# Optimization experiments

Hardware: AMD Instinct MI355X
Metric: run time of the kernel (lower is better)

The kernel has to match this reference:

```python
import jax, jax.numpy as jnp
import numpy as np

B, L, H, E = 32, 128, 768, 64


def setup_inputs() -> dict:
    key = jax.random.key(0)
    ks = jax.random.split(key, 9)
    bert = jax.random.normal(ks[0], (B, L, H), jnp.float32)
    dep = jax.random.normal(ks[1], (B, L, L, E), jnp.float32)
    adj = jax.random.bernoulli(ks[2], 0.06, (B, L, L)).astype(jnp.int32)
    adj = adj.at[:, :, L - 1].set(0)  # avoid torch.roll wrap pairing edge case
    asp_start = jax.random.randint(ks[3], (B,), 1, L // 2)
    span = jax.random.randint(ks[4], (B,), 0, 4)
    asp_end = jnp.minimum(asp_start + span, L - 2)
    sc = 1.0 / np.sqrt(H).astype(np.float32)
    Wz = jax.random.normal(ks[5], (H, H), jnp.float32) * sc
    bz = jnp.zeros((H,), jnp.float32)
    wa = jax.random.normal(ks[6], (2 * H + E,), jnp.float32) * sc
    ba = jnp.zeros((), jnp.float32)
    Wf = jax.random.normal(ks[7], (H, H + E), jnp.float32) * sc
    Wh = jax.random.normal(ks[8], (H, 2 * H), jnp.float32) * sc
    return dict(bert_hidden_states=bert, dep_type_adj=dep, deprel_adj=adj,
                asp_start=asp_start, asp_end=asp_end,
                Wz=Wz, bz=bz, wa=wa, ba=ba, Wf=Wf, Wh=Wh)


def _forward(bert, dep, adj, asp_start, asp_end, Wz, bz, wa, ba, Wf, Wh):
    # z = z_linear(bert); zs[b, j] = z[b, j+1] (rolled-mask offset: adjacency idx j -> token j+1)
    z = bert @ Wz.T + bz
    zs = jnp.roll(z, -1, axis=1)                      # [B,L,H]
    wa_i, wa_j, wa_e = wa[:H], wa[H:2 * H], wa[2 * H:]
    s_i = zs @ wa_i                                    # [B,L] current-aspect term
    s_j = zs @ wa_j                                    # [B,L] neighbor term
    s_e = jnp.einsum('bije,e->bij', dep, wa_e)         # [B,L,L] dep-embed term
    score = jax.nn.leaky_relu(s_i[:, :, None] + s_j[:, None, :] + s_e + ba, 0.01)
    nb_mask = adj > 0                                  # [B,L,L]
    attn = jax.nn.softmax(jnp.where(nb_mask, score, -1e9), axis=-1)
    attn = jnp.where(nb_mask, attn, 0.0)
    # dep_type_fusion([neighbor, dep]) = zs @ Wf_z^T + dep @ Wf_e^T; weighted sum over j
    A = zs @ Wf[:, :H].T                               # [B,L,H]
    D = jnp.einsum('bij,bije->bie', attn, dep)         # [B,L,E]
    neighbor_repr = jnp.einsum('bij,bjh->bih', attn, A) + D @ Wf[:, H:].T  # [B,L,H]
    # w_h([neighbor_repr, current_asp_repr])
    temp = neighbor_repr @ Wh[:, :H].T + zs @ Wh[:, H:].T                   # [B,L,H]
    pos = jnp.arange(L)
    asp_valid = (pos[None, :] >= asp_start[:, None]) & (pos[None, :] <= asp_end[:, None])
    upd = asp_valid & nb_mask.any(-1)                  # update only aspects with >=1 neighbor
    # result for adjacency index i is written to token position i+1
    out = jnp.where(jnp.roll(upd, 1, axis=1)[:, :, None], jnp.roll(temp, 1, axis=1), bert)
    return out


def reference(bert_hidden_states, dep_type_adj, deprel_adj, asp_start, asp_end, Wz, bz, wa, ba, Wf, Wh):
    return _forward(bert_hidden_states, dep_type_adj, deprel_adj, asp_start, asp_end,
                    Wz, bz, wa, ba, Wf, Wh)
```

## Files before the change

kernel.cpp:

```cpp
#include <hip/hip_runtime.h>
#include <math.h>

#define NB 32
#define NL 128
#define NH 768
#define NE 64

#define OFF_ASLOT   32784
#define OFF_AIDX    49168
#define OFF_NASP    49680
#define OFF_AJCNT   49808
#define OFF_AJIDX   50320
#define OFF_RMAP    148624
#define OFF_BZD     155280
#define OFF_YB      155296
#define OFF_DG      548512
#define OFF_YP      581280
#define OFF_ZSAP    2154144
#define OFF_NBR     3727008
#define OFF_VIP     6872736
#define OFF_VJP     6897312

__global__ __launch_bounds__(256) void kA(
    const int* __restrict__ adj, const int* __restrict__ asp_s, const int* __restrict__ asp_e,
    const float* __restrict__ Wz, const float* __restrict__ wa, const float* __restrict__ bz,
    const float* __restrict__ bert,
    int* __restrict__ aspect_slot, int* __restrict__ aspect_idx, int* __restrict__ nasp,
    int* __restrict__ aj_cnt, int* __restrict__ aj_idx, int* __restrict__ row_map,
    float* __restrict__ viP, float* __restrict__ vjP, float* __restrict__ bzd,
    float* __restrict__ out) {
  int blk = blockIdx.x, tid = threadIdx.x;
  if (blk < 32) {
    int b = blk;
    __shared__ int asp_flag[128];
    __shared__ int s_aidx[4];
    __shared__ int s_nasp;
    if (tid < 128) {
      const int* arow = adj + ((size_t)(b * 128 + tid)) * 128;
      int any = 0;
      for (int j = 0; j < 128; j += 4) {
        int4 v = *(const int4*)(arow + j);
        any |= v.x | v.y | v.z | v.w;
      }
      int s0 = asp_s[b], e0 = asp_e[b];
      asp_flag[tid] = (tid >= s0 && tid <= e0 && any > 0) ? 1 : 0;
      aspect_slot[b * 128 + tid] = -1;
    }
    if (tid >= 128 && tid < 132) row_map[b * 4 + (tid - 128)] = b * 128;
    __syncthreads();
    if (tid == 0) {
      int n = 0;
      for (int i = 0; i < 128; ++i)
        if (asp_flag[i] && n < 4) s_aidx[n++] = i;
      s_nasp = n;
      nasp[b] = n;
    }
    __syncthreads();
    int w = tid >> 6, l = tid & 63;
    if (w < s_nasp) {
      int a = s_aidx[w];
      if (l == 0) {
        aspect_idx[b * 4 + w] = a;
        aspect_slot[b * 128 + a] = w;
        row_map[b * 4 + w] = b * 128 + a;
      }
      const int* ar = adj + ((size_t)(b * 128 + a)) * 128;
      int v0 = (ar[l] > 0) ? 1 : 0;
      int v1 = (ar[l + 64] > 0) ? 1 : 0;
      unsigned long long m0 = __ballot(v0);
      unsigned long long m1 = __ballot(v1);
      unsigned long long below = (1ull << l) - 1ull;
      int c0 = __popcll(m0 & below);
      int c1 = __popcll(m0) + __popcll(m1 & below);
      int* dst = aj_idx + (size_t)(b * 4 + w) * 128;
      if (v0) dst[c0] = l;
      if (v1) dst[c1] = l + 64;
      if (l == 0) aj_cnt[b * 4 + w] = __popcll(m0) + __popcll(m1);
    }
  } else if (blk < 56) {
    int idx = blk - 32;
    int kb = idx % 3, hb = idx / 3;
    int k = kb * 256 + tid;
    int h0 = hb * 96;
    float ai = 0.f, aj = 0.f;
#pragma unroll 8
    for (int h = h0; h < h0 + 96; ++h) {
      float w = Wz[(size_t)h * 768 + k];
      ai += w * wa[h];
      aj += w * wa[768 + h];
    }
    viP[hb * 768 + k] = ai;
    vjP[hb * 768 + k] = aj;
  } else if (blk == 56) {
    if (tid < 64) {
      float bi = 0.f, bj = 0.f;
#pragma unroll
      for (int q = 0; q < 12; ++q) {
        float bv = bz[q * 64 + tid];
        bi += bv * wa[q * 64 + tid];
        bj += bv * wa[768 + q * 64 + tid];
      }
#pragma unroll
      for (int d = 32; d; d >>= 1) { bi += __shfl_xor(bi, d, 64); bj += __shfl_xor(bj, d, 64); }
      if (tid == 0) { bzd[0] = bi; bzd[1] = bj; }
    }
  } else {
    int row = blk - 57;
    int b = row >> 7, i = row & 127;
    __shared__ int s_upd;
    if (tid == 0) s_upd = 0;
    __syncthreads();
    if (i > 0) {
      int ip = i - 1;
      int s0 = asp_s[b], e0 = asp_e[b];
      if (ip >= s0 && ip <= e0 && tid < 64) {
        const int2* ar = (const int2*)(adj + ((size_t)(b * 128 + ip)) * 128);
        int2 v = ar[tid];
        unsigned long long m = __ballot((v.x | v.y) != 0);
        if (tid == 0 && m != 0ull) s_upd = 1;
      }
    }
    __syncthreads();
    if (tid < 192) {
      float4 v = make_float4(0.f, 0.f, 0.f, 0.f);
      if (!s_upd) v = ((const float4*)bert)[(size_t)row * 192 + tid];
      ((float4*)out)[(size_t)row * 192 + tid] = v;
    }
  }
}

__global__ __launch_bounds__(256) void kB(
    const float* __restrict__ dep, const float* __restrict__ bert,
    const float* __restrict__ wa, const float* __restrict__ ba,
    const float* __restrict__ viP, const float* __restrict__ vjP, const float* __restrict__ bzd,
    const float* __restrict__ Wz, const float* __restrict__ bz,
    const int* __restrict__ nasp, const int* __restrict__ aspect_idx,
    const int* __restrict__ aj_cnt, const int* __restrict__ aj_idx,
    const int* __restrict__ row_map,
    float* __restrict__ YB, float* __restrict__ DG, float* __restrict__ zsap) {
  int blk = blockIdx.x, tid = threadIdx.x;
  if (blk < 32) {
    int b = blk;
    int na = nasp[b];
    if (na == 0) return;
    __shared__ float vis[768];
    __shared__ float vjs[768];
    __shared__ float att[4][128];
    __shared__ float sjs[4][128];
    __shared__ float sis[4];
    __shared__ int jl[4][128];
    __shared__ int aidx[4];
    __shared__ int ajc[4];
    __shared__ float wae[64];
    if (tid < 4) { aidx[tid] = aspect_idx[b * 4 + tid]; ajc[tid] = aj_cnt[b * 4 + tid]; }
    if (tid < 64) wae[tid] = wa[1536 + tid];
    for (int q = tid; q < 512; q += 256) jl[q >> 7][q & 127] = aj_idx[b * 512 + q];
    for (int q = tid; q < 768; q += 256) {
      float a = 0.f, c = 0.f;
#pragma unroll
      for (int hb = 0; hb < 8; ++hb) { a += viP[hb * 768 + q]; c += vjP[hb * 768 + q]; }
      vis[q] = a;
      vjs[q] = c;
    }
    __syncthreads();
    int w = tid >> 6, l = tid & 63;
    float bzd0 = bzd[0], bzd1 = bzd[1];
    int offs[5];
    {
      int o = 0;
      for (int w2 = 0; w2 < 4; ++w2) { offs[w2] = o; if (w2 < na) o += 1 + ajc[w2]; }
      offs[4] = o;
    }
    for (int p = w; p < offs[4]; p += 4) {
      int w2 = 0;
      if (p >= offs[1]) w2 = 1;
      if (p >= offs[2]) w2 = 2;
      if (p >= offs[3]) w2 = 3;
      int idx = p - offs[w2];
      int row = (idx == 0) ? aidx[w2] : jl[w2][idx - 1];
      const float* br = bert + (size_t)(b * 128 + ((row + 1) & 127)) * 768;
      float acc = 0.f;
      if (idx == 0) {
#pragma unroll
        for (int q = 0; q < 12; ++q) acc += br[q * 64 + l] * vis[q * 64 + l];
      } else {
#pragma unroll
        for (int q = 0; q < 12; ++q) acc += br[q * 64 + l] * vjs[q * 64 + l];
      }
#pragma unroll
      for (int d = 32; d; d >>= 1) acc += __shfl_xor(acc, d, 64);
      if (l == 0) {
        if (idx == 0) sis[w2] = acc + bzd0;
        else sjs[w2][idx - 1] = acc + bzd1;
      }
    }
    __syncthreads();
    if (w >= na) return;
    int a = aidx[w], cj = ajc[w];
    float sib = sis[w] + ba[0];
    const float* depa = dep + ((size_t)(b * 128 + a)) * 128 * 64;
    float sc0 = -INFINITY, sc1 = -INFINITY;
    for (int t = l; t < cj; t += 64) {
      int j = jl[w][t];
      const float4* dp = (const float4*)(depa + (size_t)j * 64);
      float se = 0.f;
#pragma unroll
      for (int q = 0; q < 16; ++q) {
        float4 v = dp[q];
        se += v.x * wae[4 * q] + v.y * wae[4 * q + 1] + v.z * wae[4 * q + 2] + v.w * wae[4 * q + 3];
      }
      float sc = sib + sjs[w][t] + se;
      sc = (sc >= 0.f) ? sc : 0.01f * sc;
      if (t < 64) sc0 = sc; else sc1 = sc;
    }
    float mx = fmaxf(sc0, sc1);
#pragma unroll
    for (int d = 32; d; d >>= 1) mx = fmaxf(mx, __shfl_xor(mx, d, 64));
    float p0 = expf(sc0 - mx), p1 = expf(sc1 - mx);
    float sm = p0 + p1;
#pragma unroll
    for (int d = 32; d; d >>= 1) sm += __shfl_xor(sm, d, 64);
    float inv = 1.f / sm;
    if (l < cj) att[w][l] = p0 * inv;
    if (l + 64 < cj) att[w][l + 64] = p1 * inv;
    float y[12];
#pragma unroll
    for (int q = 0; q < 12; ++q) y[q] = 0.f;
    float dacc = 0.f;
    for (int t = 0; t < cj; ++t) {
      float at = att[w][t];
      int j = jl[w][t];
      const float* br = bert + (size_t)(b * 128 + ((j + 1) & 127)) * 768;
#pragma unroll
      for (int q = 0; q < 12; ++q) y[q] += at * br[q * 64 + l];
      dacc += at * depa[(size_t)j * 64 + l];
    }
    float* yr = YB + (size_t)(b * 4 + w) * 768;
#pragma unroll
    for (int q = 0; q < 12; ++q) yr[q * 64 + l] = y[q];
    DG[(b * 4 + w) * 64 + l] = dacc;
  } else {
    int idx = blk - 32;
    int kc = idx & 3, hc = (idx >> 2) % 3, bx = idx / 12;
    int s0 = bx * 4;
    __shared__ float Xs[4][192];
    if (tid < 192) {
      int r = tid / 48, c = tid - r * 48;
      int zrow = row_map[s0 + r];
      int bb = zrow >> 7, ii = zrow & 127;
      const float4* src = (const float4*)(bert + ((size_t)(bb * 128) + ((ii + 1) & 127)) * 768) + kc * 48;
      ((float4*)Xs[r])[c] = src[c];
    }
    __syncthreads();
    int h = hc * 256 + tid;
    const float4* wp = (const float4*)(Wz + (size_t)h * 768) + kc * 48;
    float accA[4] = {};
    float accB[4] = {};
#pragma unroll 6
    for (int k4 = 0; k4 < 24; ++k4) {
      float4 w0 = wp[k4];
      float4 w1 = wp[k4 + 24];
#pragma unroll
      for (int r = 0; r < 4; ++r) {
        float4 x0 = ((const float4*)Xs[r])[k4];
        float4 x1 = ((const float4*)Xs[r])[k4 + 24];
        accA[r] += x0.x * w0.x + x0.y * w0.y + x0.z * w0.z + x0.w * w0.w;
        accB[r] += x1.x * w1.x + x1.y * w1.y + x1.z * w1.z + x1.w * w1.w;
      }
    }
    float bzv = (kc == 0) ? bz[h] : 0.f;
#pragma unroll
    for (int r = 0; r < 4; ++r)
      zsap[((size_t)kc * 128 + s0 + r) * 768 + h] = accA[r] + accB[r] + bzv;
  }
}

__global__ __launch_bounds__(256) void kC(
    const float* __restrict__ YB, const float* __restrict__ DG, const float* __restrict__ zsap,
    const float* __restrict__ Wz, const float* __restrict__ bz,
    const float* __restrict__ Wf, const float* __restrict__ Wh,
    const int* __restrict__ row_map, const int* __restrict__ nasp,
    float* __restrict__ yp, float* __restrict__ NBR, float* __restrict__ out) {
  int blk = blockIdx.x, tid = threadIdx.x;
  __shared__ float Xs[4][192];
  if (blk < 384) {
    int kc = blk & 3, hc = (blk >> 2) % 3, bx = blk / 12;
    int s0 = bx * 4;
    if (tid < 192) {
      int r = tid / 48, c = tid - r * 48;
      const float4* src = (const float4*)(YB + (size_t)(s0 + r) * 768) + kc * 48;
      ((float4*)Xs[r])[c] = src[c];
    }
    __syncthreads();
    int h = hc * 256 + tid;
    const float4* wp = (const float4*)(Wz + (size_t)h * 768) + kc * 48;
    float accA[4] = {};
    float accB[4] = {};
#pragma unroll 6
    for (int k4 = 0; k4 < 24; ++k4) {
      float4 w0 = wp[k4];
      float4 w1 = wp[k4 + 24];
#pragma unroll
      for (int r = 0; r < 4; ++r) {
        float4 x0 = ((const float4*)Xs[r])[k4];
        float4 x1 = ((const float4*)Xs[r])[k4 + 24];
        accA[r] += x0.x * w0.x + x0.y * w0.y + x0.z * w0.z + x0.w * w0.w;
        accB[r] += x1.x * w1.x + x1.y * w1.y + x1.z * w1.z + x1.w * w1.w;
      }
    }
    float bzv = (kc == 0) ? bz[h] : 0.f;
#pragma unroll
    for (int r = 0; r < 4; ++r)
      yp[((size_t)kc * 128 + s0 + r) * 768 + h] = accA[r] + accB[r] + bzv;
  } else if (blk < 768) {
    int idx = blk - 384;
    int kc2 = idx & 3, nc = (idx >> 2) % 3, g = idx / 12;
    if (tid < 192) {
      int r = tid / 48, c = tid - r * 48;
      int row = g * 4 + r;
      int Q = kc2 * 48 + c;
      float4 p0 = *((const float4*)(zsap + (size_t)row * 768) + Q);
      float4 p1 = *((const float4*)(zsap + ((size_t)128 + row) * 768) + Q);
      float4 p2 = *((const float4*)(zsap + ((size_t)256 + row) * 768) + Q);
      float4 p3 = *((const float4*)(zsap + ((size_t)384 + row) * 768) + Q);
      ((float4*)Xs[r])[c] = make_float4(p0.x + p1.x + p2.x + p3.x, p0.y + p1.y + p2.y + p3.y,
                                        p0.z + p1.z + p2.z + p3.z, p0.w + p1.w + p2.w + p3.w);
    }
    __syncthreads();
    int h = nc * 256 + tid;
    float acc[4] = {};
    const float4* wp = (const float4*)(Wh + (size_t)h * 1536 + 768 + kc2 * 192);
#pragma unroll 4
    for (int k4 = 0; k4 < 48; ++k4) {
      float4 wv = wp[k4];
#pragma unroll
      for (int r = 0; r < 4; ++r) {
        float4 xv = ((const float4*)Xs[r])[k4];
        acc[r] += xv.x * wv.x + xv.y * wv.y + xv.z * wv.z + xv.w * wv.w;
      }
    }
#pragma unroll
    for (int r = 0; r < 4; ++r) {
      int row = g * 4 + r;
      int b = row >> 2, s = row & 3;
      if (s < nasp[b]) {
        int orow = row_map[row] + 1;
        atomicAdd(&out[(size_t)orow * 768 + h], acc[r]);
      }
    }
  } else {
    int idx = blk - 768;
    int nc = idx % 3, g = idx / 3;
    if (tid < 64) {
      int r = tid / 16, c = tid - r * 16;
      ((float4*)Xs[r])[c] = *((const float4*)(DG + (size_t)(g * 4 + r) * 64) + c);
    }
    __syncthreads();
    int h = nc * 256 + tid;
    float acc[4] = {};
    const float4* wp = (const float4*)(Wf + (size_t)h * 832 + 768);
#pragma unroll
    for (int k4 = 0; k4 < 16; ++k4) {
      float4 wv = wp[k4];
#pragma unroll
      for (int r = 0; r < 4; ++r) {
        float4 xv = ((const float4*)Xs[r])[k4];
        acc[r] += xv.x * wv.x + xv.y * wv.y + xv.z * wv.z + xv.w * wv.w;
      }
    }
#pragma unroll
    for (int r = 0; r < 4; ++r)
      NBR[(size_t)(g * 4 + r) * 768 + h] = acc[r];
  }
}

__global__ __launch_bounds__(256) void kD(
    const float* __restrict__ yp, const float* __restrict__ Wf,
    float* __restrict__ NBR) {
  int blk = blockIdx.x, tid = threadIdx.x;
  int kc = blk & 3, nc = (blk >> 2) % 3, g = blk / 12;
  __shared__ float Xs[4][192];
  if (tid < 192) {
    int r = tid / 48, c = tid - r * 48;
    int row = g * 4 + r;
    int Q = kc * 48 + c;
    float4 p0 = *((const float4*)(yp + (size_t)row * 768) + Q);
    float4 p1 = *((const float4*)(yp + ((size_t)128 + row) * 768) + Q);
    float4 p2 = *((const float4*)(yp + ((size_t)256 + row) * 768) + Q);
    float4 p3 = *((const float4*)(yp + ((size_t)384 + row) * 768) + Q);
    ((float4*)Xs[r])[c] = make_float4(p0.x + p1.x + p2.x + p3.x, p0.y + p1.y + p2.y + p3.y,
                                      p0.z + p1.z + p2.z + p3.z, p0.w + p1.w + p2.w + p3.w);
  }
  __syncthreads();
  int h = nc * 256 + tid;
  float acc[4] = {};
  const float4* wp = (const float4*)(Wf + (size_t)h * 832 + kc * 192);
#pragma unroll 4
  for (int k4 = 0; k4 < 48; ++k4) {
    float4 wv = wp[k4];
#pragma unroll
    for (int r = 0; r < 4; ++r) {
      float4 xv = ((const float4*)Xs[r])[k4];
      acc[r] += xv.x * wv.x + xv.y * wv.y + xv.z * wv.z + xv.w * wv.w;
    }
  }
#pragma unroll
  for (int r = 0; r < 4; ++r)
    atomicAdd(&NBR[(size_t)(g * 4 + r) * 768 + h], acc[r]);
}

__global__ __launch_bounds__(256) void kE(
    const float* __restrict__ NBR, const float* __restrict__ Wh,
    const int* __restrict__ row_map, const int* __restrict__ nasp,
    float* __restrict__ out) {
  int blk = blockIdx.x, tid = threadIdx.x;
  int kc = blk & 3, nc = (blk >> 2) % 3, g = blk / 12;
  __shared__ float Xs[4][192];
  if (tid < 192) {
    int r = tid / 48, c = tid - r * 48;
    ((float4*)Xs[r])[c] = *((const float4*)(NBR + (size_t)(g * 4 + r) * 768 + kc * 192) + c);
  }
  __syncthreads();
  int h = nc * 256 + tid;
  float acc[4] = {};
  const float4* wp = (const float4*)(Wh + (size_t)h * 1536 + kc * 192);
#pragma unroll 4
  for (int k4 = 0; k4 < 48; ++k4) {
    float4 wv = wp[k4];
#pragma unroll
    for (int r = 0; r < 4; ++r) {
      float4 xv = ((const float4*)Xs[r])[k4];
      acc[r] += xv.x * wv.x + xv.y * wv.y + xv.z * wv.z + xv.w * wv.w;
    }
  }
#pragma unroll
  for (int r = 0; r < 4; ++r) {
    int row = g * 4 + r;
    int b = row >> 2, s = row & 3;
    if (s < nasp[b]) {
      int orow = row_map[row] + 1;
      atomicAdd(&out[(size_t)orow * 768 + h], acc[r]);
    }
  }
}

extern "C" void kernel_launch(void* const* d_in, const int* in_sizes, int n_in,
                              void* d_out, int out_size, void* d_ws, size_t ws_size,
                              hipStream_t stream) {
  const float* bert = (const float*)d_in[0];
  const float* dep  = (const float*)d_in[1];
  const int*   adj  = (const int*)d_in[2];
  const int*   asps = (const int*)d_in[3];
  const int*   aspe = (const int*)d_in[4];
  const float* Wz   = (const float*)d_in[5];
  const float* bz   = (const float*)d_in[6];
  const float* wa   = (const float*)d_in[7];
  const float* ba   = (const float*)d_in[8];
  const float* Wf   = (const float*)d_in[9];
  const float* Wh   = (const float*)d_in[10];
  float* out = (float*)d_out;
  char* ws = (char*)d_ws;

  int*   aspect_slot = (int*)(ws + OFF_ASLOT);
  int*   aspect_idx  = (int*)(ws + OFF_AIDX);
  int*   nasp        = (int*)(ws + OFF_NASP);
  int*   aj_cnt      = (int*)(ws + OFF_AJCNT);
  int*   aj_idx      = (int*)(ws + OFF_AJIDX);
  int*   row_map     = (int*)(ws + OFF_RMAP);
  float* bzd         = (float*)(ws + OFF_BZD);
  float* YB          = (float*)(ws + OFF_YB);
  float* DG          = (float*)(ws + OFF_DG);
  float* yp          = (float*)(ws + OFF_YP);
  float* zsap        = (float*)(ws + OFF_ZSAP);
  float* NBR         = (float*)(ws + OFF_NBR);
  float* viP         = (float*)(ws + OFF_VIP);
  float* vjP         = (float*)(ws + OFF_VJP);

  kA<<<4153, 256, 0, stream>>>(adj, asps, aspe, Wz, wa, bz, bert,
                               aspect_slot, aspect_idx, nasp, aj_cnt, aj_idx, row_map,
                               viP, vjP, bzd, out);
  kB<<<416, 256, 0, stream>>>(dep, bert, wa, ba, viP, vjP, bzd, Wz, bz,
                              nasp, aspect_idx, aj_cnt, aj_idx, row_map,
                              YB, DG, zsap);
  kC<<<864, 256, 0, stream>>>(YB, DG, zsap, Wz, bz, Wf, Wh, row_map, nasp, yp, NBR, out);
  kD<<<384, 256, 0, stream>>>(yp, Wf, NBR);
  kE<<<384, 256, 0, stream>>>(NBR, Wh, row_map, nasp, out);
}
```

Baseline: 86.80 us.

## Precompose weight matrices to collapse the Wz-Wf-Wh GEMM chain into one

Multiplies the linear weights together inside the kernels: Wt = Wf_z·Wz, We = Wh_n·Wt, plus a composed dep-embedding matrix and bias vectors. Each aspect row now needs one GEMM against We instead of the YB→Wz→Wf→Wh chain. This removes two kernel launches and the intermediate yp/NBR buffers. The cost is two dense 768×768×768 weight-weight GEMMs recomputed on every call, which is far more arithmetic than the original work on about 128 rows, and the changed summation order alters rounding.

```diff
diff --git a/kernel.cpp b/kernel.cpp
--- a/kernel.cpp
+++ b/kernel.cpp
@@ -15,19 +15,23 @@
 #define OFF_BZD     155280
 #define OFF_YB      155296
 #define OFF_DG      548512
-#define OFF_YP      581280
 #define OFF_ZSAP    2154144
-#define OFF_NBR     3727008
 #define OFF_VIP     6872736
 #define OFF_VJP     6897312
+#define OFF_WT      6921888
+#define OFF_WE      9281184
+#define OFF_WDT     11640480
+#define OFF_UP      12427296
+#define OFF_C1      12439584
 
 __global__ __launch_bounds__(256) void kA(
     const int* __restrict__ adj, const int* __restrict__ asp_s, const int* __restrict__ asp_e,
     const float* __restrict__ Wz, const float* __restrict__ wa, const float* __restrict__ bz,
-    const float* __restrict__ bert,
+    const float* __restrict__ bert, const float* __restrict__ Wf, const float* __restrict__ Wh,
     int* __restrict__ aspect_slot, int* __restrict__ aspect_idx, int* __restrict__ nasp,
     int* __restrict__ aj_cnt, int* __restrict__ aj_idx, int* __restrict__ row_map,
     float* __restrict__ viP, float* __restrict__ vjP, float* __restrict__ bzd,
+    float* __restrict__ uP, float* __restrict__ Wt, float* __restrict__ Wdtp,
     float* __restrict__ out) {
   int blk = blockIdx.x, tid = threadIdx.x;
   if (blk < 32) {
@@ -71,10 +75,10 @@
       unsigned long long m1 = __ballot(v1);
       unsigned long long below = (1ull << l) - 1ull;
       int c0 = __popcll(m0 & below);
-      int c1 = __popcll(m0) + __popcll(m1 & below);
+      int c1x = __popcll(m0) + __popcll(m1 & below);
       int* dst = aj_idx + (size_t)(b * 4 + w) * 128;
       if (v0) dst[c0] = l;
-      if (v1) dst[c1] = l + 64;
+      if (v1) dst[c1x] = l + 64;
       if (l == 0) aj_cnt[b * 4 + w] = __popcll(m0) + __popcll(m1);
     }
   } else if (blk < 56) {
@@ -104,8 +108,66 @@
       for (int d = 32; d; d >>= 1) { bi += __shfl_xor(bi, d, 64); bj += __shfl_xor(bj, d, 64); }
       if (tid == 0) { bzd[0] = bi; bzd[1] = bj; }
     }
+  } else if (blk < 69) {
+    int idx = blk - 57;
+    int hc = idx >> 2, kc = idx & 3;
+    int hh = hc * 256 + tid;
+    const float4* wp = (const float4*)(Wf + (size_t)hh * 832 + kc * 192);
+    const float4* bp = (const float4*)(bz + kc * 192);
+    float acc = 0.f;
+#pragma unroll 4
+    for (int k4 = 0; k4 < 48; ++k4) {
+      float4 w = wp[k4];
+      float4 b4 = bp[k4];
+      acc += w.x * b4.x + w.y * b4.y + w.z * b4.z + w.w * b4.w;
+    }
+    uP[kc * 768 + hh] = acc;
+  } else if (blk < 357) {
+    __shared__ float Xs8[8][768];
+    int idx = blk - 69;
+    int mg = idx / 3, nc = idx % 3;
+    int m0 = mg * 8;
+    for (int q = tid; q < 8 * 768; q += 256) {
+      int r = q / 768, c = q - r * 768;
+      Xs8[r][c] = Wf[(size_t)(m0 + r) * 832 + c];
+    }
+    __syncthreads();
+    int kg = tid & 63, wv = tid >> 6;
+    int mA = wv * 2, mB = wv * 2 + 1;
+    int n4 = nc * 256 + kg * 4;
+    float4 a0 = make_float4(0.f, 0.f, 0.f, 0.f);
+    float4 a1 = make_float4(0.f, 0.f, 0.f, 0.f);
+#pragma unroll 4
+    for (int h = 0; h < 768; ++h) {
+      float4 wz = *(const float4*)(Wz + (size_t)h * 768 + n4);
+      float x0 = Xs8[mA][h], x1 = Xs8[mB][h];
+      a0.x += x0 * wz.x; a0.y += x0 * wz.y; a0.z += x0 * wz.z; a0.w += x0 * wz.w;
+      a1.x += x1 * wz.x; a1.y += x1 * wz.y; a1.z += x1 * wz.z; a1.w += x1 * wz.w;
+    }
+    *(float4*)(Wt + (size_t)(m0 + mA) * 768 + n4) = a0;
+    *(float4*)(Wt + (size_t)(m0 + mB) * 768 + n4) = a1;
+  } else if (blk < 549) {
+    __shared__ float XsW[16][192];
+    int idx = blk - 357;
+    int mgd = idx >> 2, kc = idx & 3;
+    int m0 = mgd * 16;
+    for (int q = tid; q < 16 * 192; q += 256) {
+      int r = q / 192, c = q - r * 192;
+      XsW[r][c] = Wh[(size_t)(m0 + r) * 1536 + kc * 192 + c];
+    }
+    __syncthreads();
+    int e = tid & 63, mq = tid >> 6;
+    float acc[4] = {};
+    for (int h = 0; h < 192; ++h) {
+      float wf = Wf[(size_t)(kc * 192 + h) * 832 + 768 + e];
+#pragma unroll
+      for (int j = 0; j < 4; ++j) acc[j] += XsW[mq * 4 + j][h] * wf;
+    }
+#pragma unroll
+    for (int j = 0; j < 4; ++j)
+      Wdtp[((size_t)kc * 64 + e) * 768 + m0 + mq * 4 + j] = acc[j];
   } else {
-    int row = blk - 57;
+    int row = blk - 549;
     int b = row >> 7, i = row & 127;
     __shared__ int s_upd;
     if (tid == 0) s_upd = 0;
@@ -133,11 +195,13 @@
     const float* __restrict__ dep, const float* __restrict__ bert,
     const float* __restrict__ wa, const float* __restrict__ ba,
     const float* __restrict__ viP, const float* __restrict__ vjP, const float* __restrict__ bzd,
-    const float* __restrict__ Wz, const float* __restrict__ bz,
+    const float* __restrict__ Wz, const float* __restrict__ bz, const float* __restrict__ Wh,
+    const float* __restrict__ Wt, const float* __restrict__ uP,
     const int* __restrict__ nasp, const int* __restrict__ aspect_idx,
     const int* __restrict__ aj_cnt, const int* __restrict__ aj_idx,
     const int* __restrict__ row_map,
-    float* __restrict__ YB, float* __restrict__ DG, float* __restrict__ zsap) {
+    float* __restrict__ YB, float* __restrict__ DG, float* __restrict__ zsap,
+    float* __restrict__ We, float* __restrict__ c1) {
   int blk = blockIdx.x, tid = threadIdx.x;
   if (blk < 32) {
     int b = blk;
@@ -239,11 +303,11 @@
 #pragma unroll
     for (int q = 0; q < 12; ++q) yr[q * 64 + l] = y[q];
     DG[(b * 4 + w) * 64 + l] = dacc;
-  } else {
+  } else if (blk < 416) {
+    __shared__ float Xs[4][192];
     int idx = blk - 32;
     int kc = idx & 3, hc = (idx >> 2) % 3, bx = idx / 12;
     int s0 = bx * 4;
-    __shared__ float Xs[4][192];
     if (tid < 192) {
       int r = tid / 48, c = tid - r * 48;
       int zrow = row_map[s0 + r];
@@ -272,48 +336,59 @@
 #pragma unroll
     for (int r = 0; r < 4; ++r)
       zsap[((size_t)kc * 128 + s0 + r) * 768 + h] = accA[r] + accB[r] + bzv;
+  } else if (blk < 704) {
+    __shared__ float Xs8[8][768];
+    int idx = blk - 416;
+    int mg = idx / 3, nc = idx % 3;
+    int m0 = mg * 8;
+    for (int q = tid; q < 8 * 768; q += 256) {
+      int r = q / 768, c = q - r * 768;
+      Xs8[r][c] = Wh[(size_t)(m0 + r) * 1536 + c];
+    }
+    __syncthreads();
+    int kg = tid & 63, wv = tid >> 6;
+    int mA = wv * 2, mB = wv * 2 + 1;
+    int n4 = nc * 256 + kg * 4;
+    float4 a0 = make_float4(0.f, 0.f, 0.f, 0.f);
+    float4 a1 = make_float4(0.f, 0.f, 0.f, 0.f);
+#pragma unroll 4
+    for (int h = 0; h < 768; ++h) {
+      float4 wt = *(const float4*)(Wt + (size_t)h * 768 + n4);
+      float x0 = Xs8[mA][h], x1 = Xs8[mB][h];
+      a0.x += x0 * wt.x; a0.y += x0 * wt.y; a0.z += x0 * wt.z; a0.w += x0 * wt.w;
+      a1.x += x1 * wt.x; a1.y += x1 * wt.y; a1.z += x1 * wt.z; a1.w += x1 * wt.w;
+    }
+    *(float4*)(We + (size_t)(m0 + mA) * 768 + n4) = a0;
+    *(float4*)(We + (size_t)(m0 + mB) * 768 + n4) = a1;
+  } else {
+    __shared__ float us[768];
+    for (int q = tid; q < 768; q += 256)
+      us[q] = uP[q] + uP[768 + q] + uP[1536 + q] + uP[2304 + q];
+    __syncthreads();
+    for (int hh = tid; hh < 768; hh += 256) {
+      const float4* wp = (const float4*)(Wh + (size_t)hh * 1536);
+      float acc = 0.f;
+#pragma unroll 4
+      for (int k4 = 0; k4 < 192; ++k4) {
+        float4 w = wp[k4];
+        float4 u4 = *(const float4*)(us + k4 * 4);
+        acc += w.x * u4.x + w.y * u4.y + w.z * u4.z + w.w * u4.w;
+      }
+      c1[hh] = acc;
+    }
   }
 }
 
 __global__ __launch_bounds__(256) void kC(
     const float* __restrict__ YB, const float* __restrict__ DG, const float* __restrict__ zsap,
-    const float* __restrict__ Wz, const float* __restrict__ bz,
-    const float* __restrict__ Wf, const float* __restrict__ Wh,
+    const float* __restrict__ Wh, const float* __restrict__ We, const float* __restrict__ Wdtp,
+    const float* __restrict__ c1,
     const int* __restrict__ row_map, const int* __restrict__ nasp,
-    float* __restrict__ yp, float* __restrict__ NBR, float* __restrict__ out) {
+    float* __restrict__ out) {
   int blk = blockIdx.x, tid = threadIdx.x;
   __shared__ float Xs[4][192];
   if (blk < 384) {
-    int kc = blk & 3, hc = (blk >> 2) % 3, bx = blk / 12;
-    int s0 = bx * 4;
-    if (tid < 192) {
-      int r = tid / 48, c = tid - r * 48;
-      const float4* src = (const float4*)(YB + (size_t)(s0 + r) * 768) + kc * 48;
-      ((float4*)Xs[r])[c] = src[c];
-    }
-    __syncthreads();
-    int h = hc * 256 + tid;
-    const float4* wp = (const float4*)(Wz + (size_t)h * 768) + kc * 48;
-    float accA[4] = {};
-    float accB[4] = {};
-#pragma unroll 6
-    for (int k4 = 0; k4 < 24; ++k4) {
-      float4 w0 = wp[k4];
-      float4 w1 = wp[k4 + 24];
-#pragma unroll
-      for (int r = 0; r < 4; ++r) {
-        float4 x0 = ((const float4*)Xs[r])[k4];
-        float4 x1 = ((const float4*)Xs[r])[k4 + 24];
-        accA[r] += x0.x * w0.x + x0.y * w0.y + x0.z * w0.z + x0.w * w0.w;
-        accB[r] += x1.x * w1.x + x1.y * w1.y + x1.z * w1.z + x1.w * w1.w;
-      }
-    }
-    float bzv = (kc == 0) ? bz[h] : 0.f;
-#pragma unroll
-    for (int r = 0; r < 4; ++r)
-      yp[((size_t)kc * 128 + s0 + r) * 768 + h] = accA[r] + accB[r] + bzv;
-  } else if (blk < 768) {
-    int idx = blk - 384;
+    int idx = blk;
     int kc2 = idx & 3, nc = (idx >> 2) % 3, g = idx / 12;
     if (tid < 192) {
       int r = tid / 48, c = tid - r * 48;
@@ -348,98 +423,60 @@
         atomicAdd(&out[(size_t)orow * 768 + h], acc[r]);
       }
     }
+  } else if (blk < 768) {
+    int idx = blk - 384;
+    int kc = idx & 3, nc = (idx >> 2) % 3, g = idx / 12;
+    if (tid < 192) {
+      int r = tid / 48, c = tid - r * 48;
+      ((float4*)Xs[r])[c] = *((const float4*)(YB + (size_t)(g * 4 + r) * 768 + kc * 192) + c);
+    }
+    __syncthreads();
+    int h = nc * 256 + tid;
+    float acc[4] = {};
+    const float4* wp = (const float4*)(We + (size_t)h * 768 + kc * 192);
+#pragma unroll 4
+    for (int k4 = 0; k4 < 48; ++k4) {
+      float4 wv = wp[k4];
+#pragma unroll
+      for (int r = 0; r < 4; ++r) {
+        float4 xv = ((const float4*)Xs[r])[k4];
+        acc[r] += xv.x * wv.x + xv.y * wv.y + xv.z * wv.z + xv.w * wv.w;
+      }
+    }
+    float cb = (kc == 0) ? c1[h] : 0.f;
+#pragma unroll
+    for (int r = 0; r < 4; ++r) {
+      int row = g * 4 + r;
+      int b = row >> 2, s = row & 3;
+      if (s < nasp[b]) {
+        int orow = row_map[row] + 1;
+        atomicAdd(&out[(size_t)orow * 768 + h], acc[r] + cb);
+      }
+    }
   } else {
     int idx = blk - 768;
     int nc = idx % 3, g = idx / 3;
     if (tid < 64) {
-      int r = tid / 16, c = tid - r * 16;
-      ((float4*)Xs[r])[c] = *((const float4*)(DG + (size_t)(g * 4 + r) * 64) + c);
+#pragma unroll
+      for (int r = 0; r < 4; ++r) Xs[r][tid] = DG[(size_t)(g * 4 + r) * 64 + tid];
     }
     __syncthreads();
     int h = nc * 256 + tid;
     float acc[4] = {};
-    const float4* wp = (const float4*)(Wf + (size_t)h * 832 + 768);
-#pragma unroll
-    for (int k4 = 0; k4 < 16; ++k4) {
-      float4 wv = wp[k4];
-#pragma unroll
-      for (int r = 0; r < 4; ++r) {
-        float4 xv = ((const float4*)Xs[r])[k4];
-        acc[r] += xv.x * wv.x + xv.y * wv.y + xv.z * wv.z + xv.w * wv.w;
-      }
-    }
-#pragma unroll
-    for (int r = 0; r < 4; ++r)
-      NBR[(size_t)(g * 4 + r) * 768 + h] = acc[r];
-  }
-}
-
-__global__ __launch_bounds__(256) void kD(
-    const float* __restrict__ yp, const float* __restrict__ Wf,
-    float* __restrict__ NBR) {
-  int blk = blockIdx.x, tid = threadIdx.x;
-  int kc = blk & 3, nc = (blk >> 2) % 3, g = blk / 12;
-  __shared__ float Xs[4][192];
-  if (tid < 192) {
-    int r = tid / 48, c = tid - r * 48;
-    int row = g * 4 + r;
-    int Q = kc * 48 + c;
-    float4 p0 = *((const float4*)(yp + (size_t)row * 768) + Q);
-    float4 p1 = *((const float4*)(yp + ((size_t)128 + row) * 768) + Q);
-    float4 p2 = *((const float4*)(yp + ((size_t)256 + row) * 768) + Q);
-    float4 p3 = *((const float4*)(yp + ((size_t)384 + row) * 768) + Q);
-    ((float4*)Xs[r])[c] = make_float4(p0.x + p1.x + p2.x + p3.x, p0.y + p1.y + p2.y + p3.y,
-                                      p0.z + p1.z + p2.z + p3.z, p0.w + p1.w + p2.w + p3.w);
-  }
-  __syncthreads();
-  int h = nc * 256 + tid;
-  float acc[4] = {};
-  const float4* wp = (const float4*)(Wf + (size_t)h * 832 + kc * 192);
-#pragma unroll 4
-  for (int k4 = 0; k4 < 48; ++k4) {
-    float4 wv = wp[k4];
+    for (int e = 0; e < 64; ++e) {
+      float wd = Wdtp[(size_t)e * 768 + h] + Wdtp[(size_t)(64 + e) * 768 + h] +
+                 Wdtp[(size_t)(128 + e) * 768 + h] + Wdtp[(size_t)(192 + e) * 768 + h];
+#pragma unroll
+      for (int r = 0; r < 4; ++r) acc[r] += Xs[r][e] * wd;
+    }
 #pragma unroll
     for (int r = 0; r < 4; ++r) {
-      float4 xv = ((const float4*)Xs[r])[k4];
-      acc[r] += xv.x * wv.x + xv.y * wv.y + xv.z * wv.z + xv.w * wv.w;
-    }
-  }
-#pragma unroll
-  for (int r = 0; r < 4; ++r)
-    atomicAdd(&NBR[(size_t)(g * 4 + r) * 768 + h], acc[r]);
-}
-
-__global__ __launch_bounds__(256) void kE(
-    const float* __restrict__ NBR, const float* __restrict__ Wh,
-    const int* __restrict__ row_map, const int* __restrict__ nasp,
-    float* __restrict__ out) {
-  int blk = blockIdx.x, tid = threadIdx.x;
-  int kc = blk & 3, nc = (blk >> 2) % 3, g = blk / 12;
-  __shared__ float Xs[4][192];
-  if (tid < 192) {
-    int r = tid / 48, c = tid - r * 48;
-    ((float4*)Xs[r])[c] = *((const float4*)(NBR + (size_t)(g * 4 + r) * 768 + kc * 192) + c);
-  }
-  __syncthreads();
-  int h = nc * 256 + tid;
-  float acc[4] = {};
-  const float4* wp = (const float4*)(Wh + (size_t)h * 1536 + kc * 192);
-#pragma unroll 4
-  for (int k4 = 0; k4 < 48; ++k4) {
-    float4 wv = wp[k4];
-#pragma unroll
-    for (int r = 0; r < 4; ++r) {
-      float4 xv = ((const float4*)Xs[r])[k4];
-      acc[r] += xv.x * wv.x + xv.y * wv.y + xv.z * wv.z + xv.w * wv.w;
-    }
-  }
-#pragma unroll
-  for (int r = 0; r < 4; ++r) {
-    int row = g * 4 + r;
-    int b = row >> 2, s = row & 3;
-    if (s < nasp[b]) {
-      int orow = row_map[row] + 1;
-      atomicAdd(&out[(size_t)orow * 768 + h], acc[r]);
+      int row = g * 4 + r;
+      int b = row >> 2, s = row & 3;
+      if (s < nasp[b]) {
+        int orow = row_map[row] + 1;
+        atomicAdd(&out[(size_t)orow * 768 + h], acc[r]);
+      }
     }
   }
 }
@@ -470,19 +507,20 @@
   float* bzd         = (float*)(ws + OFF_BZD);
   float* YB          = (float*)(ws + OFF_YB);
   float* DG          = (float*)(ws + OFF_DG);
-  float* yp          = (float*)(ws + OFF_YP);
   float* zsap        = (float*)(ws + OFF_ZSAP);
-  float* NBR         = (float*)(ws + OFF_NBR);
   float* viP         = (float*)(ws + OFF_VIP);
   float* vjP         = (float*)(ws + OFF_VJP);
-
-  kA<<<4153, 256, 0, stream>>>(adj, asps, aspe, Wz, wa, bz, bert,
+  float* Wt          = (float*)(ws + OFF_WT);
+  float* We          = (float*)(ws + OFF_WE);
+  float* Wdtp        = (float*)(ws + OFF_WDT);
+  float* uP          = (float*)(ws + OFF_UP);
+  float* c1          = (float*)(ws + OFF_C1);
+
+  kA<<<4645, 256, 0, stream>>>(adj, asps, aspe, Wz, wa, bz, bert, Wf, Wh,
                                aspect_slot, aspect_idx, nasp, aj_cnt, aj_idx, row_map,
-                               viP, vjP, bzd, out);
-  kB<<<416, 256, 0, stream>>>(dep, bert, wa, ba, viP, vjP, bzd, Wz, bz,
+                               viP, vjP, bzd, uP, Wt, Wdtp, out);
+  kB<<<705, 256, 0, stream>>>(dep, bert, wa, ba, viP, vjP, bzd, Wz, bz, Wh, Wt, uP,
                               nasp, aspect_idx, aj_cnt, aj_idx, row_map,
-                              YB, DG, zsap);
-  kC<<<864, 256, 0, stream>>>(YB, DG, zsap, Wz, bz, Wf, Wh, row_map, nasp, yp, NBR, out);
-  kD<<<384, 256, 0, stream>>>(yp, Wf, NBR);
-  kE<<<384, 256, 0, stream>>>(NBR, Wh, row_map, nasp, out);
+                              YB, DG, zsap, We, c1);
+  kC<<<864, 256, 0, stream>>>(YB, DG, zsap, Wh, We, Wdtp, c1, row_map, nasp, out);
 }
```

New measurement: 208.3 us. 140% more time.

## Move bert passthrough copy from first kernel into final kernel, zero only aspect rows early

Applied to the files above, without the earlier changes.

The first kernel no longer copies all 4096 rows of bert into the output. Instead 128 small blocks zero only the output rows of updated aspects, which the later atomic accumulation needs. The bulk copy of non-updated rows moves into extra blocks of the last kernel, where it can run alongside the Wh GEMV tail. This shortens the critical first kernel. The cost is a larger final launch and repeated adjacency checks.

```diff
diff --git a/kernel.cpp b/kernel.cpp
--- a/kernel.cpp
+++ b/kernel.cpp
@@ -24,7 +24,6 @@
 __global__ __launch_bounds__(256) void kA(
     const int* __restrict__ adj, const int* __restrict__ asp_s, const int* __restrict__ asp_e,
     const float* __restrict__ Wz, const float* __restrict__ wa, const float* __restrict__ bz,
-    const float* __restrict__ bert,
     int* __restrict__ aspect_slot, int* __restrict__ aspect_idx, int* __restrict__ nasp,
     int* __restrict__ aj_cnt, int* __restrict__ aj_idx, int* __restrict__ row_map,
     float* __restrict__ viP, float* __restrict__ vjP, float* __restrict__ bzd,
@@ -105,27 +104,38 @@
       if (tid == 0) { bzd[0] = bi; bzd[1] = bj; }
     }
   } else {
-    int row = blk - 57;
-    int b = row >> 7, i = row & 127;
-    __shared__ int s_upd;
-    if (tid == 0) s_upd = 0;
-    __syncthreads();
-    if (i > 0) {
-      int ip = i - 1;
-      int s0 = asp_s[b], e0 = asp_e[b];
-      if (ip >= s0 && ip <= e0 && tid < 64) {
-        const int2* ar = (const int2*)(adj + ((size_t)(b * 128 + ip)) * 128);
-        int2 v = ar[tid];
+    int g = blk - 57;
+    int b = g >> 2, s = g & 3;
+    int s0 = asp_s[b], e0 = asp_e[b];
+    __shared__ int flags[4];
+    __shared__ int arow_sh;
+    int w = tid >> 6, l = tid & 63;
+    if (w < 4) {
+      int row = s0 + w;
+      int any = 0;
+      if (row <= e0) {
+        const int2* ar = (const int2*)(adj + ((size_t)(b * 128 + row)) * 128);
+        int2 v = ar[l];
         unsigned long long m = __ballot((v.x | v.y) != 0);
-        if (tid == 0 && m != 0ull) s_upd = 1;
-      }
-    }
-    __syncthreads();
-    if (tid < 192) {
-      float4 v = make_float4(0.f, 0.f, 0.f, 0.f);
-      if (!s_upd) v = ((const float4*)bert)[(size_t)row * 192 + tid];
-      ((float4*)out)[(size_t)row * 192 + tid] = v;
-    }
+        any = (m != 0ull) ? 1 : 0;
+      }
+      if (l == 0) flags[w] = any;
+    }
+    __syncthreads();
+    if (tid == 0) {
+      int n = 0, found = -1;
+      for (int r = 0; r < 4 && s0 + r <= e0; ++r) {
+        if (flags[r]) {
+          if (n == s) { found = s0 + r; break; }
+          ++n;
+        }
+      }
+      arow_sh = found;
+    }
+    __syncthreads();
+    int arow = arow_sh;
+    if (arow >= 0 && tid < 192)
+      ((float4*)out)[(size_t)(b * 128 + arow + 1) * 192 + tid] = make_float4(0.f, 0.f, 0.f, 0.f);
   }
 }
 
@@ -412,35 +422,58 @@
 __global__ __launch_bounds__(256) void kE(
     const float* __restrict__ NBR, const float* __restrict__ Wh,
     const int* __restrict__ row_map, const int* __restrict__ nasp,
+    const int* __restrict__ adj, const int* __restrict__ asp_s, const int* __restrict__ asp_e,
+    const float* __restrict__ bert,
     float* __restrict__ out) {
   int blk = blockIdx.x, tid = threadIdx.x;
-  int kc = blk & 3, nc = (blk >> 2) % 3, g = blk / 12;
-  __shared__ float Xs[4][192];
-  if (tid < 192) {
-    int r = tid / 48, c = tid - r * 48;
-    ((float4*)Xs[r])[c] = *((const float4*)(NBR + (size_t)(g * 4 + r) * 768 + kc * 192) + c);
-  }
-  __syncthreads();
-  int h = nc * 256 + tid;
-  float acc[4] = {};
-  const float4* wp = (const float4*)(Wh + (size_t)h * 1536 + kc * 192);
+  if (blk < 384) {
+    int kc = blk & 3, nc = (blk >> 2) % 3, g = blk / 12;
+    __shared__ float Xs[4][192];
+    if (tid < 192) {
+      int r = tid / 48, c = tid - r * 48;
+      ((float4*)Xs[r])[c] = *((const float4*)(NBR + (size_t)(g * 4 + r) * 768 + kc * 192) + c);
+    }
+    __syncthreads();
+    int h = nc * 256 + tid;
+    float acc[4] = {};
+    const float4* wp = (const float4*)(Wh + (size_t)h * 1536 + kc * 192);
 #pragma unroll 4
-  for (int k4 = 0; k4 < 48; ++k4) {
-    float4 wv = wp[k4];
+    for (int k4 = 0; k4 < 48; ++k4) {
+      float4 wv = wp[k4];
+#pragma unroll
+      for (int r = 0; r < 4; ++r) {
+        float4 xv = ((const float4*)Xs[r])[k4];
+        acc[r] += xv.x * wv.x + xv.y * wv.y + xv.z * wv.z + xv.w * wv.w;
+      }
+    }
 #pragma unroll
     for (int r = 0; r < 4; ++r) {
-      float4 xv = ((const float4*)Xs[r])[k4];
-      acc[r] += xv.x * wv.x + xv.y * wv.y + xv.z * wv.z + xv.w * wv.w;
-    }
-  }
-#pragma unroll
-  for (int r = 0; r < 4; ++r) {
-    int row = g * 4 + r;
-    int b = row >> 2, s = row & 3;
-    if (s < nasp[b]) {
-      int orow = row_map[row] + 1;
-      atomicAdd(&out[(size_t)orow * 768 + h], acc[r]);
-    }
+      int row = g * 4 + r;
+      int b = row >> 2, s = row & 3;
+      if (s < nasp[b]) {
+        int orow = row_map[row] + 1;
+        atomicAdd(&out[(size_t)orow * 768 + h], acc[r]);
+      }
+    }
+  } else {
+    int row = blk - 384;
+    int b = row >> 7, i = row & 127;
+    __shared__ int s_upd;
+    if (tid == 0) s_upd = 0;
+    __syncthreads();
+    if (i > 0) {
+      int ip = i - 1;
+      int s0 = asp_s[b], e0 = asp_e[b];
+      if (ip >= s0 && ip <= e0 && tid < 64) {
+        const int2* ar = (const int2*)(adj + ((size_t)(b * 128 + ip)) * 128);
+        int2 v = ar[tid];
+        unsigned long long m = __ballot((v.x | v.y) != 0);
+        if (tid == 0 && m != 0ull) s_upd = 1;
+      }
+    }
+    __syncthreads();
+    if (!s_upd && tid < 192)
+      ((float4*)out)[(size_t)row * 192 + tid] = ((const float4*)bert)[(size_t)row * 192 + tid];
   }
 }
 
@@ -476,13 +509,13 @@
   float* viP         = (float*)(ws + OFF_VIP);
   float* vjP         = (float*)(ws + OFF_VJP);
 
-  kA<<<4153, 256, 0, stream>>>(adj, asps, aspe, Wz, wa, bz, bert,
-                               aspect_slot, aspect_idx, nasp, aj_cnt, aj_idx, row_map,
-                               viP, vjP, bzd, out);
+  kA<<<185, 256, 0, stream>>>(adj, asps, aspe, Wz, wa, bz,
+                              aspect_slot, aspect_idx, nasp, aj_cnt, aj_idx, row_map,
+                              viP, vjP, bzd, out);
   kB<<<416, 256, 0, stream>>>(dep, bert, wa, ba, viP, vjP, bzd, Wz, bz,
                               nasp, aspect_idx, aj_cnt, aj_idx, row_map,
                               YB, DG, zsap);
   kC<<<864, 256, 0, stream>>>(YB, DG, zsap, Wz, bz, Wf, Wh, row_map, nasp, yp, NBR, out);
   kD<<<384, 256, 0, stream>>>(yp, Wf, NBR);
-  kE<<<384, 256, 0, stream>>>(NBR, Wh, row_map, nasp, out);
+  kE<<<4480, 256, 0, stream>>>(NBR, Wh, row_map, nasp, adj, asps, aspe, bert, out);
 }
```

Measured after the change: 87.08 us. About the same (+0.3%).
